# Kernel tuning notes

Hardware: AMD Instinct MI355X
Metric: run time of the kernel (lower is better)

The kernel has to match this reference:

```python
import jax, jax.numpy as jnp
import numpy as np

IN_CH = 1280
NUM_HEADS = 8
DIM_DOWN = 5
CUT_RATE = 4
SCALE = (IN_CH // NUM_HEADS) ** -0.5  # faithful to original: uses in_ch//num_heads


def setup_inputs() -> dict:
    key = jax.random.key(0)
    ks = jax.random.split(key, 5)
    B, N = 4, 4096
    C = IN_CH // DIM_DOWN  # 256
    x = jax.random.normal(ks[0], (B, N, IN_CH), dtype=jnp.float32)
    Wd = jax.random.normal(ks[1], (IN_CH, C), dtype=jnp.float32) * (IN_CH ** -0.5)
    Wqkv = jax.random.normal(ks[2], (C, 3 * C), dtype=jnp.float32) * (C ** -0.5)
    Wup = jax.random.normal(ks[3], (C, IN_CH), dtype=jnp.float32) * (C ** -0.5)
    bup = jnp.zeros((IN_CH,), dtype=jnp.float32)
    return {"x": x, "Wd": Wd, "Wqkv": Wqkv, "Wup": Wup, "bup": bup}


def reference(x, Wd, Wqkv, Wup, bup):
    # dim-down projection (dropout is identity at rate 0 / eval)
    h = x @ Wd                                  # [B, N, C]
    B, N, C = h.shape
    H = NUM_HEADS
    hd = C // H
    blk = N // CUT_RATE
    qkv = (h @ Wqkv).reshape(B, N, 3, H, hd)
    qkv = jnp.transpose(qkv, (2, 0, 3, 1, 4))   # [3, B, H, N, hd]
    q, k, v = qkv[0], qkv[1], qkv[2]
    # block-diagonal local attention: split N into CUT_RATE independent chunks
    q = q.reshape(B, H, CUT_RATE, blk, hd)
    k = k.reshape(B, H, CUT_RATE, blk, hd)
    v = v.reshape(B, H, CUT_RATE, blk, hd)
    attn = jnp.einsum('bhcqd,bhckd->bhcqk', q, k) * SCALE
    attn = jax.nn.softmax(attn, axis=-1)
    o = jnp.einsum('bhcqk,bhckd->bhcqd', attn, v)
    # torch cat over chunks along token dim, then merge heads: [B, N, C]
    o = jnp.transpose(o, (0, 2, 3, 1, 4)).reshape(B, N, C)
    return o @ Wup + bup
```

## Files before the change

### kernel.cpp

```cpp
#include <hip/hip_runtime.h>

typedef unsigned short u16;
typedef unsigned int u32;
typedef u16 u16x8 __attribute__((ext_vector_type(8)));
typedef __bf16 bf16x8 __attribute__((ext_vector_type(8)));
typedef float f32x4 __attribute__((ext_vector_type(4)));

__device__ __forceinline__ u16 f2bf(float f) {
  union { float f; unsigned u; } c; c.f = f;
  unsigned u = c.u;
  return (u16)((u + 0x7fff + ((u >> 16) & 1)) >> 16);
}

__device__ __forceinline__ float fexp2(float x) {
#if __has_builtin(__builtin_amdgcn_exp2f)
  return __builtin_amdgcn_exp2f(x);
#else
  float r; asm("v_exp_f32 %0, %1" : "=v"(r) : "v"(x)); return r;
#endif
}

__device__ __forceinline__ u32 cvtpk(float lo, float hi) {
  u32 r;
  asm("v_cvt_pk_bf16_f32 %0, %1, %2" : "=v"(r) : "v"(lo), "v"(hi));
  return r;
}

__device__ __forceinline__ void lds16(const u16* g, u16* l) {
  __builtin_amdgcn_global_load_lds(
      (const __attribute__((address_space(1))) unsigned int*)g,
      (__attribute__((address_space(3))) unsigned int*)l, 16, 0, 0);
}

#define CEXP (0.07905694150420949f * 1.4426950408889634f)

#define PREP_W (1280 * 256 + 768 * 256 + 1280 * 256)

__global__ __launch_bounds__(256)
void prep_all(const float* __restrict__ Wd, const float* __restrict__ Wqkv,
              const float* __restrict__ Wup, const float* __restrict__ X,
              u16* __restrict__ WdC, u16* __restrict__ WqkvT,
              u16* __restrict__ WupT, u16* __restrict__ Xb, int n8) {
  int id = blockIdx.x * 256 + threadIdx.x;
  if (id < 1280 * 256) {
    WdC[id] = f2bf(Wd[id]);
    return;
  }
  id -= 1280 * 256;
  if (id < 768 * 256) {
    int n = id >> 8, c = id & 255;
    float v = Wqkv[(size_t)c * 768 + n];
    if (n < 256) v *= CEXP;
    WqkvT[id] = f2bf(v);
    return;
  }
  id -= 768 * 256;
  if (id < 1280 * 256) {
    int n = id >> 8, c = id & 255;
    WupT[id] = f2bf(Wup[(size_t)c * 1280 + n]);
    return;
  }
  id -= 1280 * 256;
  if (id < n8) {
    const float4* src = (const float4*)(X + (size_t)id * 8);
    float4 lo = src[0], hi = src[1];
    u16x8 v;
    v[0]=f2bf(lo.x); v[1]=f2bf(lo.y); v[2]=f2bf(lo.z); v[3]=f2bf(lo.w);
    v[4]=f2bf(hi.x); v[5]=f2bf(hi.y); v[6]=f2bf(hi.z); v[7]=f2bf(hi.w);
    *(u16x8*)(Xb + (size_t)id * 8) = v;
  }
}

template <int AF32>
__global__ __launch_bounds__(256)
void gemm_bt(const void* __restrict__ Av,
             const u16* __restrict__ BT,
             u16* __restrict__ Cb, float* __restrict__ Cf,
             const float* __restrict__ bias,
             int M, int N, int K)
{
  __shared__ u16 As[128][64];
  __shared__ u16 Bs[128][64];
  const int tid  = threadIdx.x;
  const int wave = tid >> 6, lane = tid & 63;
  const int quad = lane >> 4, l16 = lane & 15;

  const int nb = N >> 7, mb = M >> 7;
  int band, nblk;
  if ((mb & 7) == 0) {
    int xcd = blockIdx.x & 7, slot = blockIdx.x >> 3;
    band = xcd + 8 * (slot / nb);
    nblk = slot % nb;
  } else {
    band = blockIdx.x / nb;
    nblk = blockIdx.x % nb;
  }
  const int m0 = band * 128, n0 = nblk * 128;
  const int wr = (wave >> 1) * 64, wc = (wave & 1) * 64;
  const u16*   A16 = (const u16*)Av;
  const float* A32 = (const float*)Av;

  f32x4 acc[4][4];
#pragma unroll
  for (int i = 0; i < 4; i++)
#pragma unroll
    for (int j = 0; j < 4; j++) acc[i][j] = f32x4{0.f, 0.f, 0.f, 0.f};

  for (int k0 = 0; k0 < K; k0 += 64) {
    if constexpr (AF32) {
#pragma unroll
      for (int it = 0; it < 4; it++) {
        int idx = tid + it * 256;
        int r = idx >> 3;
        int c = (idx & 7) << 3;
        const float* src = &A32[(size_t)(m0 + r) * K + k0 + c];
        float4 lo = *(const float4*)src;
        float4 hi = *(const float4*)(src + 4);
        u16x8 v;
        v[0]=f2bf(lo.x); v[1]=f2bf(lo.y); v[2]=f2bf(lo.z); v[3]=f2bf(lo.w);
        v[4]=f2bf(hi.x); v[5]=f2bf(hi.y); v[6]=f2bf(hi.z); v[7]=f2bf(hi.w);
        *(u16x8*)&As[r][c] = v;
      }
#pragma unroll
      for (int it = 0; it < 4; it++) {
        int r0 = wave * 32 + it * 8;
        lds16(&BT[(size_t)(n0 + r0 + (lane >> 3)) * K + k0 + ((lane & 7) << 3)],
              &Bs[r0][0] + lane * 8);
      }
    } else {
#pragma unroll
      for (int it = 0; it < 4; it++) {
        int r0 = wave * 32 + it * 8;
        lds16(&A16[(size_t)(m0 + r0 + (lane >> 3)) * K + k0 + ((lane & 7) << 3)],
              &As[r0][0] + lane * 8);
        lds16(&BT[(size_t)(n0 + r0 + (lane >> 3)) * K + k0 + ((lane & 7) << 3)],
              &Bs[r0][0] + lane * 8);
      }
    }
    __syncthreads();
#pragma unroll
    for (int ks = 0; ks < 64; ks += 32) {
      bf16x8 af[4], bfr[4];
#pragma unroll
      for (int i = 0; i < 4; i++)
        af[i] = *(const bf16x8*)&As[wr + i * 16 + l16][ks + quad * 8];
#pragma unroll
      for (int j = 0; j < 4; j++)
        bfr[j] = *(const bf16x8*)&Bs[wc + j * 16 + l16][ks + quad * 8];
#pragma unroll
      for (int i = 0; i < 4; i++)
#pragma unroll
        for (int j = 0; j < 4; j++)
          acc[i][j] = __builtin_amdgcn_mfma_f32_16x16x32_bf16(af[i], bfr[j], acc[i][j], 0, 0, 0);
    }
    __syncthreads();
  }

#pragma unroll
  for (int i = 0; i < 4; i++) {
#pragma unroll
    for (int j = 0; j < 4; j++) {
      int col = n0 + wc + j * 16 + l16;
      float bv = bias ? bias[col] : 0.0f;
#pragma unroll
      for (int r = 0; r < 4; r++) {
        int row = m0 + wr + i * 16 + quad * 4 + r;
        float v = acc[i][j][r] + bv;
        if (Cf) Cf[(size_t)row * N + col] = v;
        else    Cb[(size_t)row * N + col] = f2bf(v);
      }
    }
  }
}

__global__ __launch_bounds__(512, 2)
void gemm_bt256(const u16* __restrict__ A16, const u16* __restrict__ BT,
                u16* __restrict__ Cb, int M, int N, int K)
{
  __shared__ __align__(16) u16 As[4][256][32];
  __shared__ __align__(16) u16 Bs[4][256][32];
  const int tid  = threadIdx.x;
  const int wave = tid >> 6, lane = tid & 63;
  const int quad = lane >> 4, l16 = lane & 15;
  const int wm = wave >> 2, wn = wave & 3;

  const int nb = N >> 8, mb = M >> 8;
  int band, nblk;
  if ((mb & 7) == 0) {
    int xcd = blockIdx.x & 7, slot = blockIdx.x >> 3;
    band = xcd + 8 * (slot / nb);
    nblk = slot % nb;
  } else {
    band = blockIdx.x / nb;
    nblk = blockIdx.x % nb;
  }
  const int m0 = band * 256, n0 = nblk * 256;
  const int nt = K >> 5;

  const int r0a = tid >> 2;
  const int r1a = r0a + 128;
  const int c8  = (tid & 3) << 3;
  const int o0  = tid * 8;
  const int o1  = o0 + 512 * 8;

  auto stage = [&](int t) {
    const int b = t & 3;
    const int k0 = t << 5;
    lds16(&A16[(size_t)(m0 + r0a) * K + k0 + c8], (u16*)As[b] + o0);
    lds16(&A16[(size_t)(m0 + r1a) * K + k0 + c8], (u16*)As[b] + o1);
    lds16(&BT [(size_t)(n0 + r0a) * K + k0 + c8], (u16*)Bs[b] + o0);
    lds16(&BT [(size_t)(n0 + r1a) * K + k0 + c8], (u16*)Bs[b] + o1);
  };

  f32x4 acc[8][4];
#pragma unroll
  for (int i = 0; i < 8; i++)
#pragma unroll
    for (int j = 0; j < 4; j++) acc[i][j] = f32x4{0.f, 0.f, 0.f, 0.f};

  stage(0); stage(1); stage(2);
  asm volatile("s_waitcnt vmcnt(8)" ::: "memory");
  __builtin_amdgcn_s_barrier();
  asm volatile("" ::: "memory");

  for (int t = 0; t < nt; ++t) {
    const int b = t & 3;
    if (t + 3 < nt) stage(t + 3);

    bf16x8 af[8], bf[4];
#pragma unroll
    for (int i = 0; i < 8; i++)
      af[i] = *(const bf16x8*)&As[b][wm * 128 + i * 16 + l16][quad * 8];
#pragma unroll
    for (int j = 0; j < 4; j++)
      bf[j] = *(const bf16x8*)&Bs[b][wn * 64 + j * 16 + l16][quad * 8];

    __builtin_amdgcn_s_setprio(1);
#pragma unroll
    for (int i = 0; i < 8; i++)
#pragma unroll
      for (int j = 0; j < 4; j++)
        acc[i][j] = __builtin_amdgcn_mfma_f32_16x16x32_bf16(af[i], bf[j], acc[i][j], 0, 0, 0);
    __builtin_amdgcn_s_setprio(0);

    if (t + 1 < nt) {
      const int last = (t + 3 < nt) ? (t + 3) : (nt - 1);
      const int pend = last - (t + 1);
      if (pend >= 2)      asm volatile("s_waitcnt vmcnt(8)" ::: "memory");
      else if (pend == 1) asm volatile("s_waitcnt vmcnt(4)" ::: "memory");
      else                asm volatile("s_waitcnt vmcnt(0)" ::: "memory");
      __builtin_amdgcn_s_barrier();
      asm volatile("" ::: "memory");
    }
  }

#pragma unroll
  for (int i = 0; i < 8; i++) {
#pragma unroll
    for (int j = 0; j < 4; j++) {
      const int col = n0 + wn * 64 + j * 16 + l16;
#pragma unroll
      for (int r = 0; r < 4; r++) {
        const int row = m0 + wm * 128 + i * 16 + quad * 4 + r;
        Cb[(size_t)row * N + col] = f2bf(acc[i][j][r]);
      }
    }
  }
}

__global__ __launch_bounds__(256)
void vtrans(const u16* __restrict__ qkv, u16* __restrict__ vT)
{
  __shared__ u16 T[32][72];
  const int tid   = threadIdx.x;
  const int kt    = blockIdx.x;
  const int head  = blockIdx.y >> 2;
  const int chunk = blockIdx.y & 3;
  const int b     = blockIdx.z;
  const size_t rowbase = (size_t)b * 4096 + chunk * 1024 + kt * 64;

  const int tok = tid >> 2;
  const int d8  = (tid & 3) << 3;
  u16x8 vv = *(const u16x8*)&qkv[(rowbase + tok) * 768 + 512 + head * 32 + d8];
  const int rot = (tok + (d8 >> 3)) & 7;
#pragma unroll
  for (int jj = 0; jj < 8; jj++) {
    int j = (jj + rot) & 7;
    T[d8 + j][tok] = vv[j];
  }
  __syncthreads();
  const int d = tid >> 3;
  const int s = tid & 7;
  u16x8 out = *(const u16x8*)&T[d][s * 8];
  size_t obase = ((size_t)((b * 4 + chunk) * 8 + head)) * 32768
               + (size_t)d * 1024 + kt * 64 + s * 8;
  *(u16x8*)&vT[obase] = out;
}

__global__ __launch_bounds__(256)
void attn_kernel(const u16* __restrict__ qkv, const u16* __restrict__ vT,
                 u16* __restrict__ o)
{
  __shared__ __align__(16) u16 Ks[2][64][32];
  __shared__ __align__(16) u16 VTs[2][32][64];
  __shared__ u16 Ps[4][32][72];

  const int tid  = threadIdx.x;
  const int wave = tid >> 6, lane = tid & 63;
  const int quad = lane >> 4, l16 = lane & 15;
  const int qb    = blockIdx.x;
  const int head  = blockIdx.y >> 2;
  const int chunk = blockIdx.y & 3;
  const int b     = blockIdx.z;
  const size_t rowbase = (size_t)b * 4096 + chunk * 1024;
  const int tok0 = qb * 128 + wave * 32;

  const int kkey = tid >> 2;
  const int kd8  = (tid & 3) << 3;
  const int vr   = tid >> 3;
  const int vs   = tid & 7;
  const int vsl  = (vs ^ (vr & 7)) << 3;
  const size_t vbase = ((size_t)((b * 4 + chunk) * 8 + head)) * 32768
                     + (size_t)vr * 1024 + vsl;

  auto stageKV = [&](int kb, int buf) {
    lds16(&qkv[(rowbase + kb * 64 + kkey) * 768 + 256 + head * 32 + kd8],
          &Ks[buf][0][0] + tid * 8);
    lds16(&vT[vbase + (size_t)kb * 64], &VTs[buf][0][0] + tid * 8);
  };

  stageKV(0, 0);

  bf16x8 qf[2];
#pragma unroll
  for (int qt = 0; qt < 2; qt++)
    qf[qt] = *(const bf16x8*)&qkv[(rowbase + tok0 + qt * 16 + l16) * 768 + head * 32 + quad * 8];

  float lsum[2] = {0.f, 0.f};
  f32x4 Oacc[2][2];
#pragma unroll
  for (int qt = 0; qt < 2; qt++)
#pragma unroll
    for (int nd = 0; nd < 2; nd++) Oacc[qt][nd] = f32x4{0.f, 0.f, 0.f, 0.f};

  __syncthreads();

  for (int kb = 0; kb < 16; kb++) {
    const int cur = kb & 1;
    if (kb < 15) stageKV(kb + 1, cur ^ 1);

    bf16x8 kf[4];
#pragma unroll
    for (int kt = 0; kt < 4; kt++)
      kf[kt] = *(const bf16x8*)&Ks[cur][kt * 16 + l16][quad * 8];

    f32x4 ST[4][2];
    __builtin_amdgcn_s_setprio(1);
#pragma unroll
    for (int kt = 0; kt < 4; kt++)
#pragma unroll
      for (int qt = 0; qt < 2; qt++)
        ST[kt][qt] = __builtin_amdgcn_mfma_f32_16x16x32_bf16(kf[kt], qf[qt], f32x4{0.f,0.f,0.f,0.f}, 0, 0, 0);
    __builtin_amdgcn_s_setprio(0);

#pragma unroll
    for (int qt = 0; qt < 2; qt++) {
#pragma unroll
      for (int kt = 0; kt < 4; kt++) {
        float p0 = fexp2(ST[kt][qt][0]);
        float p1 = fexp2(ST[kt][qt][1]);
        float p2 = fexp2(ST[kt][qt][2]);
        float p3 = fexp2(ST[kt][qt][3]);
        lsum[qt] += (p0 + p1) + (p2 + p3);
        uint2 dd;
        dd.x = cvtpk(p0, p1);
        dd.y = cvtpk(p2, p3);
        *(uint2*)&Ps[wave][qt * 16 + l16][kt * 16 + quad * 4] = dd;
      }
    }

#pragma unroll
    for (int ks = 0; ks < 2; ks++) {
      bf16x8 vf[2], pf[2];
#pragma unroll
      for (int nd = 0; nd < 2; nd++)
        vf[nd] = *(const bf16x8*)&VTs[cur][nd * 16 + l16][((ks * 4 + quad) ^ (l16 & 7)) << 3];
#pragma unroll
      for (int qt = 0; qt < 2; qt++)
        pf[qt] = *(const bf16x8*)&Ps[wave][qt * 16 + l16][ks * 32 + quad * 8];
      __builtin_amdgcn_s_setprio(1);
#pragma unroll
      for (int qt = 0; qt < 2; qt++)
#pragma unroll
        for (int nd = 0; nd < 2; nd++)
          Oacc[qt][nd] = __builtin_amdgcn_mfma_f32_16x16x32_bf16(pf[qt], vf[nd], Oacc[qt][nd], 0, 0, 0);
      __builtin_amdgcn_s_setprio(0);
    }

    __syncthreads();
  }

#pragma unroll
  for (int qt = 0; qt < 2; qt++) {
    float s = lsum[qt];
    s += __shfl_xor(s, 16);
    s += __shfl_xor(s, 32);
    lsum[qt] = s;
  }
#pragma unroll
  for (int qt = 0; qt < 2; qt++)
#pragma unroll
    for (int r = 0; r < 4; r++) {
      float inv = 1.0f / __shfl(lsum[qt], quad * 4 + r, 16);
      size_t row = rowbase + tok0 + qt * 16 + quad * 4 + r;
#pragma unroll
      for (int nd = 0; nd < 2; nd++) {
        int col = head * 32 + nd * 16 + l16;
        o[row * 256 + col] = f2bf(Oacc[qt][nd][r] * inv);
      }
    }
}

extern "C" void kernel_launch(void* const* d_in, const int* in_sizes, int n_in,
                              void* d_out, int out_size, void* d_ws, size_t ws_size,
                              hipStream_t stream)
{
  const float* x    = (const float*)d_in[0];
  const float* Wd   = (const float*)d_in[1];
  const float* Wqkv = (const float*)d_in[2];
  const float* Wup  = (const float*)d_in[3];
  const float* bup  = (const float*)d_in[4];
  float* out = (float*)d_out;

  const int M = 4 * 4096;

  u16* WdC   = (u16*)d_ws;
  u16* WqkvT = WdC   + 1280 * 256;
  u16* WupT  = WqkvT + 768 * 256;
  u16* WpT   = WupT  + 1280 * 256;
  u16* qkv   = WpT   + 768 * 1280;
  u16* ob    = qkv   + (size_t)M * 768;
  u16* xb    = ob    + (size_t)M * 256;
  u16* vT    = xb;

  const size_t need = ((size_t)(1280*256 + 768*256 + 1280*256 + 768*1280)
                       + (size_t)M * (768 + 256 + 1280)) * sizeof(u16);
  const bool use_xb = ws_size >= need;

  const int n8 = use_xb ? (M * 1280 / 8) : 0;
  prep_all<<<(PREP_W + n8 + 255) / 256, 256, 0, stream>>>(
      Wd, Wqkv, Wup, x, WdC, WqkvT, WupT, xb, n8);

  gemm_bt<0><<<dim3((1280 / 128) * (768 / 128)), 256, 0, stream>>>(
      (const void*)WqkvT, WdC, WpT, nullptr, nullptr, 768, 1280, 256);

  if (use_xb) {
    gemm_bt256<<<dim3((768 / 256) * (M / 256)), 512, 0, stream>>>(
        xb, WpT, qkv, M, 768, 1280);
  } else {
    gemm_bt<1><<<dim3((768 / 128) * (M / 128)), 256, 0, stream>>>(
        (const void*)x, WpT, qkv, nullptr, nullptr, M, 768, 1280);
  }

  vtrans<<<dim3(16, 32, 4), 256, 0, stream>>>(qkv, vT);

  attn_kernel<<<dim3(8, 32, 4), 256, 0, stream>>>(qkv, vT, ob);

  gemm_bt<0><<<dim3((1280 / 128) * (M / 128)), 256, 0, stream>>>(
      (const void*)ob, WupT, nullptr, out, bup, M, 1280, 256);
}
```

Measured before the change: 298.4 us.

## Add XOR LDS swizzle and restructure 256-tile GEMM into ping-pong staged pipeline

Adds an XOR swizzle to the LDS layouts of both GEMM kernels so that MFMA fragment reads avoid bank conflicts. The 256x256 GEMM moves from a 4-deep K=32 ring buffer to a double-buffered K=64 layout split into 128-row halves. Loads are staged in quarter-tile pieces interleaved with four MFMA sub-blocks separated by barriers, in a ping-pong schedule. It also hard-codes v_exp_f32 for exp2. The extra barriers and the more complex schedule could add synchronization overhead, and correctness depends on the vmcnt counts matching the number of outstanding loads.

```diff
diff --git a/kernel.cpp b/kernel.cpp
--- a/kernel.cpp
+++ b/kernel.cpp
@@ -13,11 +13,7 @@
 }
 
 __device__ __forceinline__ float fexp2(float x) {
-#if __has_builtin(__builtin_amdgcn_exp2f)
-  return __builtin_amdgcn_exp2f(x);
-#else
   float r; asm("v_exp_f32 %0, %1" : "=v"(r) : "v"(x)); return r;
-#endif
 }
 
 __device__ __forceinline__ u32 cvtpk(float lo, float hi) {
@@ -84,6 +80,8 @@
   const int tid  = threadIdx.x;
   const int wave = tid >> 6, lane = tid & 63;
   const int quad = lane >> 4, l16 = lane & 15;
+  const int rsw  = l16 & 7;
+  const int ssw  = ((lane & 7) ^ (lane >> 3)) << 3;
 
   const int nb = N >> 7, mb = M >> 7;
   int band, nblk;
@@ -112,28 +110,27 @@
       for (int it = 0; it < 4; it++) {
         int idx = tid + it * 256;
         int r = idx >> 3;
-        int c = (idx & 7) << 3;
-        const float* src = &A32[(size_t)(m0 + r) * K + k0 + c];
+        const float* src = &A32[(size_t)(m0 + r) * K + k0 + ((idx & 7) << 3)];
         float4 lo = *(const float4*)src;
         float4 hi = *(const float4*)(src + 4);
         u16x8 v;
         v[0]=f2bf(lo.x); v[1]=f2bf(lo.y); v[2]=f2bf(lo.z); v[3]=f2bf(lo.w);
         v[4]=f2bf(hi.x); v[5]=f2bf(hi.y); v[6]=f2bf(hi.z); v[7]=f2bf(hi.w);
-        *(u16x8*)&As[r][c] = v;
+        *(u16x8*)&As[r][((idx & 7) ^ (r & 7)) << 3] = v;
       }
 #pragma unroll
       for (int it = 0; it < 4; it++) {
         int r0 = wave * 32 + it * 8;
-        lds16(&BT[(size_t)(n0 + r0 + (lane >> 3)) * K + k0 + ((lane & 7) << 3)],
+        lds16(&BT[(size_t)(n0 + r0 + (lane >> 3)) * K + k0 + ssw],
               &Bs[r0][0] + lane * 8);
       }
     } else {
 #pragma unroll
       for (int it = 0; it < 4; it++) {
         int r0 = wave * 32 + it * 8;
-        lds16(&A16[(size_t)(m0 + r0 + (lane >> 3)) * K + k0 + ((lane & 7) << 3)],
+        lds16(&A16[(size_t)(m0 + r0 + (lane >> 3)) * K + k0 + ssw],
               &As[r0][0] + lane * 8);
-        lds16(&BT[(size_t)(n0 + r0 + (lane >> 3)) * K + k0 + ((lane & 7) << 3)],
+        lds16(&BT[(size_t)(n0 + r0 + (lane >> 3)) * K + k0 + ssw],
               &Bs[r0][0] + lane * 8);
       }
     }
@@ -143,10 +140,10 @@
       bf16x8 af[4], bfr[4];
 #pragma unroll
       for (int i = 0; i < 4; i++)
-        af[i] = *(const bf16x8*)&As[wr + i * 16 + l16][ks + quad * 8];
+        af[i] = *(const bf16x8*)&As[wr + i * 16 + l16][(((ks >> 3) + quad) ^ rsw) << 3];
 #pragma unroll
       for (int j = 0; j < 4; j++)
-        bfr[j] = *(const bf16x8*)&Bs[wc + j * 16 + l16][ks + quad * 8];
+        bfr[j] = *(const bf16x8*)&Bs[wc + j * 16 + l16][(((ks >> 3) + quad) ^ rsw) << 3];
 #pragma unroll
       for (int i = 0; i < 4; i++)
 #pragma unroll
@@ -173,16 +170,39 @@
   }
 }
 
+#define BAR()  do { asm volatile("" ::: "memory"); \
+                    __builtin_amdgcn_s_barrier(); \
+                    asm volatile("" ::: "memory"); } while (0)
+#define VMC(n) asm volatile("s_waitcnt vmcnt(" #n ")" ::: "memory")
+
+#define LDA_(d, ib) { _Pragma("unroll") for (int i = 0; i < 4; i++) \
+  _Pragma("unroll") for (int ks = 0; ks < 2; ks++) \
+    af[i*2+ks] = *(const bf16x8*)&As[d][wm][(ib+i)*16 + l16][((ks*4+quad) ^ rsw) << 3]; }
+
+#define LDB_(d, dst, jp) { _Pragma("unroll") for (int j = 0; j < 2; j++) \
+  _Pragma("unroll") for (int ks = 0; ks < 2; ks++) \
+    dst[j*2+ks] = *(const bf16x8*)&Bs[d][bh][br + (jp*2+j)*16 + l16][((ks*4+quad) ^ rsw) << 3]; }
+
+#define MM_(ib, jp, breg) { __builtin_amdgcn_s_setprio(1); \
+  _Pragma("unroll") for (int i = 0; i < 4; i++) \
+  _Pragma("unroll") for (int j = 0; j < 2; j++) \
+  _Pragma("unroll") for (int ks = 0; ks < 2; ks++) \
+    acc[ib+i][jp*2+j] = __builtin_amdgcn_mfma_f32_16x16x32_bf16( \
+        af[i*2+ks], breg[j*2+ks], acc[ib+i][jp*2+j], 0, 0, 0); \
+  __builtin_amdgcn_s_setprio(0); }
+
 __global__ __launch_bounds__(512, 2)
 void gemm_bt256(const u16* __restrict__ A16, const u16* __restrict__ BT,
                 u16* __restrict__ Cb, int M, int N, int K)
 {
-  __shared__ __align__(16) u16 As[4][256][32];
-  __shared__ __align__(16) u16 Bs[4][256][32];
+  __shared__ __align__(16) u16 As[2][2][128][64];
+  __shared__ __align__(16) u16 Bs[2][2][128][64];
   const int tid  = threadIdx.x;
   const int wave = tid >> 6, lane = tid & 63;
   const int quad = lane >> 4, l16 = lane & 15;
   const int wm = wave >> 2, wn = wave & 3;
+  const int bh = wn >> 1, br = (wn & 1) * 64;
+  const int rsw = l16 & 7;
 
   const int nb = N >> 8, mb = M >> 8;
   int band, nblk;
@@ -195,62 +215,69 @@
     nblk = blockIdx.x % nb;
   }
   const int m0 = band * 256, n0 = nblk * 256;
-  const int nt = K >> 5;
-
-  const int r0a = tid >> 2;
-  const int r1a = r0a + 128;
-  const int c8  = (tid & 3) << 3;
-  const int o0  = tid * 8;
-  const int o1  = o0 + 512 * 8;
-
-  auto stage = [&](int t) {
-    const int b = t & 3;
-    const int k0 = t << 5;
-    lds16(&A16[(size_t)(m0 + r0a) * K + k0 + c8], (u16*)As[b] + o0);
-    lds16(&A16[(size_t)(m0 + r1a) * K + k0 + c8], (u16*)As[b] + o1);
-    lds16(&BT [(size_t)(n0 + r0a) * K + k0 + c8], (u16*)Bs[b] + o0);
-    lds16(&BT [(size_t)(n0 + r1a) * K + k0 + c8], (u16*)Bs[b] + o1);
+  const int NT = K >> 6;
+
+  const int srow = tid >> 3;
+  const int scol = ((tid & 7) ^ (srow & 7)) << 3;
+
+  auto stageA = [&](int t, int h) {
+    const int d = t & 1;
+    const size_t g = (size_t)(m0 + h * 128 + srow) * K + (t << 6) + scol;
+    lds16(&A16[g], &As[d][h][0][0] + tid * 8);
+    lds16(&A16[g + (size_t)64 * K], &As[d][h][64][0] + tid * 8);
   };
-
+  auto stageB = [&](int t, int h) {
+    const int d = t & 1;
+    const size_t g = (size_t)(n0 + h * 128 + srow) * K + (t << 6) + scol;
+    lds16(&BT[g], &Bs[d][h][0][0] + tid * 8);
+    lds16(&BT[g + (size_t)64 * K], &Bs[d][h][64][0] + tid * 8);
+  };
+
+  bf16x8 af[8], b0[4], b1[4];
   f32x4 acc[8][4];
 #pragma unroll
   for (int i = 0; i < 8; i++)
 #pragma unroll
     for (int j = 0; j < 4; j++) acc[i][j] = f32x4{0.f, 0.f, 0.f, 0.f};
 
-  stage(0); stage(1); stage(2);
-  asm volatile("s_waitcnt vmcnt(8)" ::: "memory");
-  __builtin_amdgcn_s_barrier();
-  asm volatile("" ::: "memory");
-
-  for (int t = 0; t < nt; ++t) {
-    const int b = t & 3;
-    if (t + 3 < nt) stage(t + 3);
-
-    bf16x8 af[8], bf[4];
-#pragma unroll
-    for (int i = 0; i < 8; i++)
-      af[i] = *(const bf16x8*)&As[b][wm * 128 + i * 16 + l16][quad * 8];
-#pragma unroll
-    for (int j = 0; j < 4; j++)
-      bf[j] = *(const bf16x8*)&Bs[b][wn * 64 + j * 16 + l16][quad * 8];
-
-    __builtin_amdgcn_s_setprio(1);
-#pragma unroll
-    for (int i = 0; i < 8; i++)
-#pragma unroll
-      for (int j = 0; j < 4; j++)
-        acc[i][j] = __builtin_amdgcn_mfma_f32_16x16x32_bf16(af[i], bf[j], acc[i][j], 0, 0, 0);
-    __builtin_amdgcn_s_setprio(0);
-
-    if (t + 1 < nt) {
-      const int last = (t + 3 < nt) ? (t + 3) : (nt - 1);
-      const int pend = last - (t + 1);
-      if (pend >= 2)      asm volatile("s_waitcnt vmcnt(8)" ::: "memory");
-      else if (pend == 1) asm volatile("s_waitcnt vmcnt(4)" ::: "memory");
-      else                asm volatile("s_waitcnt vmcnt(0)" ::: "memory");
-      __builtin_amdgcn_s_barrier();
-      asm volatile("" ::: "memory");
+  stageA(0, 0); stageA(0, 1); stageB(0, 0); stageB(0, 1); stageA(1, 0);
+  VMC(2);
+  BAR();
+
+  const int nIter = NT >> 1;
+  for (int it = 0; it < nIter; ++it) {
+    const int t0 = it * 2, t1 = t0 + 1;
+    const bool more  = (t0 + 2 < NT);
+    const bool more1 = (t1 + 2 < NT);
+
+    LDA_(0, 0); LDB_(0, b0, 0);
+    stageA(t1, 1);
+    BAR(); MM_(0, 0, b0); BAR();
+    LDB_(0, b1, 1);
+    stageB(t1, 0);
+    BAR(); MM_(0, 1, b1); BAR();
+    LDA_(0, 4);
+    stageB(t1, 1);
+    BAR(); MM_(4, 1, b1); BAR();
+    if (more) stageA(t0 + 2, 0);
+    BAR(); MM_(4, 0, b0);
+    if (more) { VMC(2); } else { VMC(0); }
+    BAR();
+
+    LDA_(1, 0); LDB_(1, b0, 0);
+    if (more) stageA(t0 + 2, 1);
+    BAR(); MM_(0, 0, b0); BAR();
+    LDB_(1, b1, 1);
+    if (more) stageB(t0 + 2, 0);
+    BAR(); MM_(0, 1, b1); BAR();
+    LDA_(1, 4);
+    if (more) stageB(t0 + 2, 1);
+    BAR(); MM_(4, 1, b1); BAR();
+    if (more1) stageA(t1 + 2, 0);
+    BAR(); MM_(4, 0, b0);
+    if (it + 1 < nIter) {
+      if (more1) { VMC(2); } else { VMC(0); }
+      BAR();
     }
   }
 
```

Result: faster. 277.5 us (-7.0%).
